# Kernel optimization log

Measured on AMD Instinct MI355X. Metric: run time of the kernel, lower is better.

The kernel has to match this reference:

```python
import jax, jax.numpy as jnp
import numpy as np

B, D, H, O, C, L = 16384, 1024, 1024, 256, 8, 3  # batch, input, hidden, output, num_classes, num_layers


def setup_inputs() -> dict:
    key = jax.random.key(0)
    ks = jax.random.split(key, 9)
    s_in = 1.0 / np.sqrt(D)
    s_h = 1.0 / np.sqrt(H)
    return {
        "x": jax.random.normal(ks[0], (B, D), jnp.float32),
        # classifier: Linear(D, C)
        "Wc": jax.random.normal(ks[1], (D, C), jnp.float32) * s_in,
        "bc": jnp.zeros((C,), jnp.float32),
        # per-branch first linear: Linear(D, H), stacked over C branches
        "W1": jax.random.normal(ks[2], (C, D, H), jnp.float32) * s_in,
        "b1": jnp.zeros((C, H), jnp.float32),
        # per-branch hidden linears: (num_layers-1) x Linear(H, H)
        "W2": jax.random.normal(ks[3], (C, L - 1, H, H), jnp.float32) * s_h,
        "b2": jnp.zeros((C, L - 1, H), jnp.float32),
        # per-branch output linear: Linear(H, O)
        "Wo": jax.random.normal(ks[4], (C, H, O), jnp.float32) * s_h,
        "bo": jnp.zeros((C, O), jnp.float32),
    }


def reference(x, Wc, bc, W1, b1, W2, b2, Wo, bo):
    # classifier logits: (B, C)
    logits = x @ Wc + bc
    # argmax routing (no target_bin given), clamped as in torch
    class_idx = jnp.clip(jnp.argmax(logits, axis=-1), 0, C - 1)
    one_hot = jax.nn.one_hot(class_idx, C, dtype=x.dtype)  # (B, C)
    # dense compute-all-branches, faithful to the torch module
    h = jax.nn.relu(jnp.einsum("bd,cdh->bch", x, W1) + b1)  # (B, C, H)
    for i in range(L - 1):
        h = jax.nn.relu(jnp.einsum("bch,chk->bck", h, W2[:, i]) + b2[:, i])
    outputs = jnp.einsum("bch,cho->bco", h, Wo) + bo  # (B, C, O)
    output = jnp.sum(one_hot[:, :, None] * outputs, axis=1)  # (B, O)
    return output, logits
```

## Files before the change

kernel.cpp:

```cpp
#include <hip/hip_runtime.h>
#include <stdint.h>

#define BB 16384
#define DD 1024
#define HH 1024
#define OO 256
#define CC 8

typedef unsigned short u16;
typedef __attribute__((ext_vector_type(4))) unsigned short u16x4;
typedef __attribute__((ext_vector_type(8))) short bf16x8;
typedef __attribute__((ext_vector_type(4))) float f32x4;

__device__ __forceinline__ u16 f2bf(float f) {
    union { float f; uint32_t u; } v; v.f = f;
    const uint32_t u = v.u;
    return (u16)((u + 0x7FFFu + ((u >> 16) & 1u)) >> 16);
}

#define GLDS16(g, l)                                                                   \
    __builtin_amdgcn_global_load_lds((const __attribute__((address_space(1))) void*)(g), \
                                     (__attribute__((address_space(3))) void*)(l), 16, 0, 0)

__global__ __launch_bounds__(256)
void transpose_bf16_kernel(const float* __restrict__ src, u16* __restrict__ dst,
                           int R, int Cc)
{
    __shared__ float t[32][33];
    const int tid = threadIdx.x;
    const int mat = blockIdx.z;
    const int r0 = blockIdx.y * 32, c0 = blockIdx.x * 32;
    {
        const int rr = tid >> 3, c4 = (tid & 7) * 4;
        const float4 v = *(const float4*)(src + ((size_t)mat * R + r0 + rr) * Cc + c0 + c4);
        t[rr][c4 + 0] = v.x; t[rr][c4 + 1] = v.y; t[rr][c4 + 2] = v.z; t[rr][c4 + 3] = v.w;
    }
    __syncthreads();
    {
        const int cc = tid >> 3, k4 = (tid & 7) * 4;
        u16x4 o;
        o[0] = f2bf(t[k4 + 0][cc]);
        o[1] = f2bf(t[k4 + 1][cc]);
        o[2] = f2bf(t[k4 + 2][cc]);
        o[3] = f2bf(t[k4 + 3][cc]);
        *(u16x4*)(dst + ((size_t)mat * Cc + c0 + cc) * R + r0 + k4) = o;
    }
}

__global__ __launch_bounds__(256)
void logits_kernel(const float* __restrict__ x, const float* __restrict__ Wc,
                   const float* __restrict__ bc, float* __restrict__ logits_out,
                   u16* __restrict__ x_bf16, int* __restrict__ class_idx,
                   int* __restrict__ hist)
{
    __shared__ float WcT[CC][DD];
    __shared__ int clsarr[16];
    const int tid = threadIdx.x;
    #pragma unroll
    for (int j = 0; j < 8; ++j) {
        const int f = tid + 256 * j;
        const float4 v = ((const float4*)Wc)[f];
        const int d = f >> 1, c = (f & 1) * 4;
        WcT[c + 0][d] = v.x; WcT[c + 1][d] = v.y; WcT[c + 2][d] = v.z; WcT[c + 3][d] = v.w;
    }
    __syncthreads();

    const int lane = tid & 63, wv = tid >> 6;
    const int row0 = blockIdx.x * 16 + wv * 4;

    float acc[4][8];
    #pragma unroll
    for (int r = 0; r < 4; ++r)
        #pragma unroll
        for (int c = 0; c < 8; ++c) acc[r][c] = 0.f;

    #pragma unroll
    for (int p = 0; p < 2; ++p) {
        float4 xv[2][4];
        #pragma unroll
        for (int rr = 0; rr < 2; ++rr) {
            const float4* xr = (const float4*)(x + (size_t)(row0 + 2 * p + rr) * DD);
            #pragma unroll
            for (int j = 0; j < 4; ++j) xv[rr][j] = xr[lane + 64 * j];
        }
        #pragma unroll
        for (int rr = 0; rr < 2; ++rr) {
            u16* xb = x_bf16 + (size_t)(row0 + 2 * p + rr) * DD;
            #pragma unroll
            for (int j = 0; j < 4; ++j) {
                const float4 v = xv[rr][j];
                u16x4 o; o[0] = f2bf(v.x); o[1] = f2bf(v.y); o[2] = f2bf(v.z); o[3] = f2bf(v.w);
                *(u16x4*)(xb + 4 * (lane + 64 * j)) = o;
            }
        }
        #pragma unroll
        for (int j = 0; j < 4; ++j) {
            const int f = lane + 64 * j;
            #pragma unroll
            for (int c = 0; c < 8; ++c) {
                const float4 w = *(const float4*)&WcT[c][4 * f];
                #pragma unroll
                for (int rr = 0; rr < 2; ++rr)
                    acc[2 * p + rr][c] += xv[rr][j].x * w.x + xv[rr][j].y * w.y
                                        + xv[rr][j].z * w.z + xv[rr][j].w * w.w;
            }
        }
    }

    #pragma unroll
    for (int off = 8; off < 64; off <<= 1)
        #pragma unroll
        for (int r = 0; r < 4; ++r)
            #pragma unroll
            for (int c = 0; c < 8; ++c)
                acc[r][c] += __shfl_xor(acc[r][c], off, 64);

    const int cls = lane >> 3;
    const float bcv = bc[cls];
    float s[4];
    #pragma unroll
    for (int r = 0; r < 4; ++r) {
        float v = acc[r][0];
        #pragma unroll
        for (int c = 1; c < 8; ++c) v = (cls == c) ? acc[r][c] : v;
        s[r] = v;
    }
    #pragma unroll
    for (int off = 1; off < 8; off <<= 1)
        #pragma unroll
        for (int r = 0; r < 4; ++r) s[r] += __shfl_xor(s[r], off, 64);
    #pragma unroll
    for (int r = 0; r < 4; ++r) s[r] += bcv;

    #pragma unroll
    for (int r = 0; r < 4; ++r)
        if ((lane & 7) == 0) logits_out[(size_t)(row0 + r) * CC + cls] = s[r];

    int idx[4] = {cls, cls, cls, cls};
    #pragma unroll
    for (int off = 8; off < 64; off <<= 1) {
        #pragma unroll
        for (int r = 0; r < 4; ++r) {
            const float ov = __shfl_xor(s[r], off, 64);
            const int oi = __shfl_xor(idx[r], off, 64);
            const bool take = (ov > s[r]) || (ov == s[r] && oi < idx[r]);
            s[r] = take ? ov : s[r];
            idx[r] = take ? oi : idx[r];
        }
    }
    if (lane == 0) {
        #pragma unroll
        for (int r = 0; r < 4; ++r) {
            class_idx[row0 + r] = idx[r];
            clsarr[wv * 4 + r] = idx[r];
        }
    }
    __syncthreads();
    if (tid < 64) {
        const int myc = (tid < 16) ? clsarr[tid] : -1;
        int h = 0;
        #pragma unroll
        for (int cc = 0; cc < 8; ++cc) {
            const int p = __popcll(__ballot(myc == cc));
            h = (tid == cc) ? p : h;
        }
        if (tid < 8) hist[blockIdx.x * 8 + tid] = h;
    }
}

__global__ __launch_bounds__(256)
void scan_kernel(const int* __restrict__ hist, int* __restrict__ offsets,
                 int* __restrict__ bb)
{
    const int t = threadIdx.x, c = t >> 5, g = t & 31;
    int sum = 0;
    #pragma unroll 4
    for (int i = 0; i < 32; ++i) sum += hist[(g * 32 + i) * 8 + c];
    int inc = sum;
    #pragma unroll
    for (int d = 1; d < 32; d <<= 1) {
        const int v = __shfl_up(inc, d, 32);
        if (g >= d) inc += v;
    }
    __shared__ int tot[8], offL[9];
    if (g == 31) tot[c] = inc;
    __syncthreads();
    if (t == 0) {
        int o = 0; offL[0] = 0; offsets[0] = 0;
        #pragma unroll
        for (int c8 = 0; c8 < 8; ++c8) {
            o += (tot[c8] + 127) & ~127;
            offL[c8 + 1] = o; offsets[c8 + 1] = o;
        }
    }
    __syncthreads();
    int base = offL[c] + (inc - sum);
    #pragma unroll 4
    for (int i = 0; i < 32; ++i) {
        const int b = g * 32 + i;
        bb[b * 8 + c] = base;
        base += hist[b * 8 + c];
    }
}

__global__ __launch_bounds__(256)
void scatter_kernel(const int* __restrict__ class_idx, const int* __restrict__ bb,
                    int* __restrict__ rowidx)
{
    const int r = blockIdx.x * 256 + threadIdx.x;
    const int c = class_idx[r];
    const int lane = threadIdx.x & 63;
    const int gl = lane & ~15;
    const unsigned long long before = (1ull << lane) - (1ull << gl);
    int rank = 0;
    #pragma unroll
    for (int cc = 0; cc < 8; ++cc) {
        const unsigned long long m = __ballot(c == cc);
        const int p = __popcll(m & before);
        rank = (c == cc) ? p : rank;
    }
    rowidx[bb[(r >> 4) * 8 + c] + rank] = r;
}

#define STAGE(b, kt)                            \
    {                                           \
        const int kb_ = (kt) * 32;              \
        GLDS16(gA0 + kb_, lA0 + (b) * 4096);    \
        GLDS16(gA1 + kb_, lA1 + (b) * 4096);    \
        GLDS16(gB0 + kb_, lB0 + (b) * 4096);    \
        GLDS16(gB1 + kb_, lB1 + (b) * 4096);    \
    }

#define COMPUTE(b)                                                        \
    {                                                                     \
        bf16x8 af[4], bfr[4];                                             \
        _Pragma("unroll")                                                 \
        for (int i = 0; i < 4; ++i) {                                     \
            af[i]  = *(const bf16x8*)(fA + (b) * 4096 + i * 16 * 32);     \
            bfr[i] = *(const bf16x8*)(fB + (b) * 4096 + i * 16 * 32);     \
        }                                                                 \
        __builtin_amdgcn_s_setprio(1);                                    \
        _Pragma("unroll")                                                 \
        for (int mi = 0; mi < 4; ++mi)                                    \
            _Pragma("unroll")                                             \
            for (int ni = 0; ni < 4; ++ni)                                \
                acc[mi][ni] = __builtin_amdgcn_mfma_f32_16x16x32_bf16(    \
                    af[mi], bfr[ni], acc[mi][ni], 0, 0, 0);               \
        __builtin_amdgcn_s_setprio(0);                                    \
    }

#define WAITV(N)                                                          \
    asm volatile("s_waitcnt vmcnt(" #N ")" ::: "memory");                 \
    __builtin_amdgcn_s_barrier();                                         \
    __builtin_amdgcn_sched_barrier(0);

template<int NT_Y, int NSTRIDE, bool GATHER_A, bool RELU, bool FINAL>
__global__ __launch_bounds__(256, 3)
void gemm_kernel(const u16* __restrict__ Abase, const u16* __restrict__ Wbase,
                 size_t wclass_stride, const float* __restrict__ bias_base,
                 int bias_stride, const int* __restrict__ offsets,
                 const int* __restrict__ rowidx, u16* __restrict__ Hout,
                 float* __restrict__ Fout)
{
    __shared__ u16 sA[3 * 128 * 32];
    __shared__ u16 sB[3 * 128 * 32];
    const int tid = threadIdx.x;

    const int bid = blockIdx.x;
    const int wg = (bid & 7) * ((int)gridDim.x >> 3) + (bid >> 3);
    const int m0 = (wg / NT_Y) * 128;
    const int n0 = (wg % NT_Y) * 128;
    if (m0 >= offsets[CC]) return;
    int c = 0;
    while (m0 >= offsets[c + 1]) ++c;

    const int srow = tid >> 2;
    const int kc8 = (tid & 3) * 8;
    int sa0 = m0 + srow, sa1 = m0 + srow + 64;
    if (GATHER_A) {
        const int g0 = rowidx[sa0]; sa0 = (g0 < 0) ? 0 : g0;
        const int g1 = rowidx[sa1]; sa1 = (g1 < 0) ? 0 : g1;
    }
    const u16* gA0 = Abase + (size_t)sa0 * 1024 + kc8;
    const u16* gA1 = Abase + (size_t)sa1 * 1024 + kc8;
    const u16* Wcl = Wbase + (size_t)c * wclass_stride;
    const u16* gB0 = Wcl + (size_t)(n0 + srow) * 1024 + kc8;
    const u16* gB1 = Wcl + (size_t)(n0 + srow + 64) * 1024 + kc8;
    u16* lA0 = sA + tid * 8;
    u16* lA1 = sA + 2048 + tid * 8;
    u16* lB0 = sB + tid * 8;
    u16* lB1 = sB + 2048 + tid * 8;

    const int lane = tid & 63, wv = tid >> 6;
    const int wm = (wv & 1) * 64, wn = (wv >> 1) * 64;
    const int lr = lane & 15, lg = lane >> 4;
    const u16* fA = sA + (wm + lr) * 32 + lg * 8;
    const u16* fB = sB + (wn + lr) * 32 + lg * 8;

    f32x4 acc[4][4];
    #pragma unroll
    for (int i = 0; i < 4; ++i)
        #pragma unroll
        for (int j = 0; j < 4; ++j)
            acc[i][j] = (f32x4){0.f, 0.f, 0.f, 0.f};

    STAGE(0, 0);
    STAGE(1, 1);
    for (int kt = 0; kt < 30; kt += 3) {
        WAITV(4);
        STAGE(2, kt + 2);
        COMPUTE(0);
        WAITV(4);
        STAGE(0, kt + 3);
        COMPUTE(1);
        WAITV(4);
        STAGE(1, kt + 4);
        COMPUTE(2);
    }
    WAITV(4);
    COMPUTE(0);
    WAITV(0);
    COMPUTE(1);

    const float* bp = bias_base + (size_t)c * bias_stride + n0 + wn + lr;
    #pragma unroll
    for (int ni = 0; ni < 4; ++ni) {
        const float bv = bp[ni * 16];
        const int col = n0 + wn + ni * 16 + lr;
        #pragma unroll
        for (int mi = 0; mi < 4; ++mi) {
            const int rb = m0 + wm + mi * 16 + lg * 4;
            #pragma unroll
            for (int q = 0; q < 4; ++q) {
                float v = acc[mi][ni][q] + bv;
                if (RELU) v = v > 0.f ? v : 0.f;
                if (FINAL) {
                    const int orow = rowidx[rb + q];
                    if (orow >= 0) Fout[(size_t)orow * NSTRIDE + col] = v;
                } else {
                    Hout[(size_t)(rb + q) * NSTRIDE + col] = f2bf(v);
                }
            }
        }
    }
}

extern "C" void kernel_launch(void* const* d_in, const int* in_sizes, int n_in,
                              void* d_out, int out_size, void* d_ws, size_t ws_size,
                              hipStream_t stream)
{
    const float* x  = (const float*)d_in[0];
    const float* Wc = (const float*)d_in[1];
    const float* bc = (const float*)d_in[2];
    const float* W1 = (const float*)d_in[3];
    const float* b1 = (const float*)d_in[4];
    const float* W2 = (const float*)d_in[5];
    const float* b2 = (const float*)d_in[6];
    const float* Wo = (const float*)d_in[7];
    const float* bo = (const float*)d_in[8];
    float* out    = (float*)d_out;
    float* logits = out + (size_t)BB * OO;

    char* ws = (char*)d_ws;
    constexpr size_t PADMAX = BB + CC * 128;
    constexpr int NLB = BB / 16;
    int* offsets   = (int*)(ws + 0);
    int* hist      = (int*)(ws + 64);
    int* bb        = (int*)(ws + 64 + NLB * 32);
    int* class_idx = (int*)(ws + 64 + 2 * NLB * 32);
    int* rowidx    = (int*)((char*)class_idx + (size_t)BB * 4);
    u16* x_bf16    = (u16*)((char*)rowidx + PADMAX * 4);
    u16* hA  = x_bf16 + (size_t)BB * DD;
    u16* hB  = hA + PADMAX * HH;
    u16* W1T = hB + PADMAX * HH;
    u16* W2T = W1T + (size_t)CC * DD * HH;
    u16* WoT = W2T + (size_t)CC * 2 * HH * HH;

    hipMemsetAsync(rowidx, 0xFF, PADMAX * 4, stream);

    transpose_bf16_kernel<<<dim3(32, 32, 8),  256, 0, stream>>>(W1, W1T, DD, HH);
    transpose_bf16_kernel<<<dim3(32, 32, 16), 256, 0, stream>>>(W2, W2T, HH, HH);
    transpose_bf16_kernel<<<dim3(8, 32, 8),   256, 0, stream>>>(Wo, WoT, HH, OO);

    logits_kernel<<<NLB, 256, 0, stream>>>(x, Wc, bc, logits, x_bf16, class_idx, hist);
    scan_kernel<<<1, 256, 0, stream>>>(hist, offsets, bb);
    scatter_kernel<<<BB / 256, 256, 0, stream>>>(class_idx, bb, rowidx);

    constexpr int MT = BB / 128 + CC;
    gemm_kernel<8, HH, true,  true,  false><<<dim3(MT * 8), 256, 0, stream>>>(
        x_bf16, W1T, (size_t)DD * HH, b1, HH, offsets, rowidx, hA, nullptr);
    gemm_kernel<8, HH, false, true,  false><<<dim3(MT * 8), 256, 0, stream>>>(
        hA, W2T, (size_t)2 * HH * HH, b2, 2 * HH, offsets, rowidx, hB, nullptr);
    gemm_kernel<8, HH, false, true,  false><<<dim3(MT * 8), 256, 0, stream>>>(
        hB, W2T + (size_t)HH * HH, (size_t)2 * HH * HH, b2 + HH, 2 * HH, offsets, rowidx, hA, nullptr);
    gemm_kernel<2, OO, false, false, true ><<<dim3(MT * 2), 256, 0, stream>>>(
        hA, WoT, (size_t)OO * HH, bo, OO, offsets, rowidx, nullptr, out);
}
```

Measured before the change: 273.8 us.

## Use 256x128 tiles with warp-specialized loaders and swizzled LDS for hidden GEMMs

Replaces the 128x128 hidden-layer GEMM with a 256x128 tile kernel, padding class segments to 256 rows. Two waves load A and two load B into an XOR-swizzled LDS layout, and each wave computes a 128x64 sub-tile with 8x4 MFMA accumulators. The larger tile is meant to raise arithmetic intensity and cut per-tile weight reloads, while the swizzle targets LDS bank conflicts. The cost is more registers and lower occupancy (launch bounds of 2), plus extra padded rows per class.

```diff
diff --git a/kernel.cpp b/kernel.cpp
--- a/kernel.cpp
+++ b/kernel.cpp
@@ -189,7 +189,7 @@
         int o = 0; offL[0] = 0; offsets[0] = 0;
         #pragma unroll
         for (int c8 = 0; c8 < 8; ++c8) {
-            o += (tot[c8] + 127) & ~127;
+            o += (tot[c8] + 255) & ~255;
             offL[c8 + 1] = o; offsets[c8 + 1] = o;
         }
     }
@@ -220,6 +220,139 @@
         rank = (c == cc) ? p : rank;
     }
     rowidx[bb[(r >> 4) * 8 + c] + rank] = r;
+}
+
+#define ABUF 8192
+#define BBUF 4096
+
+template<bool GATHER_A>
+__global__ __launch_bounds__(256, 2)
+void gemm256_kernel(const u16* __restrict__ Abase, const u16* __restrict__ Wbase,
+                    size_t wclass_stride, const float* __restrict__ bias_base,
+                    int bias_stride, const int* __restrict__ offsets,
+                    const int* __restrict__ rowidx, u16* __restrict__ Hout)
+{
+    __shared__ u16 sA[3 * ABUF];
+    __shared__ u16 sB[3 * BBUF];
+    const int tid = threadIdx.x;
+
+    const int bid = blockIdx.x;
+    const int wg = (bid & 7) * ((int)gridDim.x >> 3) + (bid >> 3);
+    const int m0 = (wg >> 3) * 256;
+    const int n0 = (wg & 7) * 128;
+    if (m0 >= offsets[CC]) return;
+    int c = 0;
+    while (m0 >= offsets[c + 1]) ++c;
+
+    const int wv = tid >> 6, ln = tid & 63;
+    const bool isA = (wv == 1 || wv == 2);
+    const int nGld = isA ? 8 : 4;
+    const int chunkBase = isA ? ((wv - 1) * 512) : ((wv == 3) ? 256 : 0);
+    const int bufStep = isA ? ABUF : BBUF;
+    u16* const ldsBase = isA ? sA : sB;
+    const u16* const Wcl = Wbase + (size_t)c * wclass_stride;
+
+    const u16* gsrc[8];
+    u16* ldst[8];
+    #pragma unroll
+    for (int j = 0; j < 8; ++j) {
+        if (j < nGld) {
+            const int n = chunkBase + j * 64 + ln;
+            const int row = n >> 2;
+            const int logc = (n & 3) ^ ((row >> 1) & 3);
+            ldst[j] = ldsBase + n * 8;
+            if (isA) {
+                int grow = m0 + row;
+                if (GATHER_A) { const int g = rowidx[grow]; grow = (g < 0) ? 0 : g; }
+                gsrc[j] = Abase + (size_t)grow * 1024 + logc * 8;
+            } else {
+                gsrc[j] = Wcl + (size_t)(n0 + row) * 1024 + logc * 8;
+            }
+        } else { gsrc[j] = nullptr; ldst[j] = nullptr; }
+    }
+
+    const int wm = wv >> 1, wn = wv & 1, lr = ln & 15, lg = ln >> 4;
+    const int arow0 = wm * 128 + lr;
+    const int brow0 = wn * 64 + lr;
+    const int pcA = lg ^ ((arow0 >> 1) & 3);
+    const int pcB = lg ^ ((brow0 >> 1) & 3);
+    const u16* const fA = sA + arow0 * 32 + pcA * 8;
+    const u16* const fB = sB + brow0 * 32 + pcB * 8;
+
+    f32x4 acc[8][4];
+    #pragma unroll
+    for (int i = 0; i < 8; ++i)
+        #pragma unroll
+        for (int j = 0; j < 4; ++j)
+            acc[i][j] = (f32x4){0.f, 0.f, 0.f, 0.f};
+
+#define STAGE6(KT, P)                                                     \
+    {                                                                     \
+        _Pragma("unroll")                                                 \
+        for (int j = 0; j < 8; ++j)                                       \
+            if (j < nGld) GLDS16(gsrc[j] + (KT) * 32, ldst[j] + (P) * bufStep); \
+    }
+
+#define COMPUTE6(P)                                                       \
+    {                                                                     \
+        bf16x8 bfr[4];                                                    \
+        _Pragma("unroll")                                                 \
+        for (int ni = 0; ni < 4; ++ni)                                    \
+            bfr[ni] = *(const bf16x8*)(fB + (P) * BBUF + ni * 512);       \
+        __builtin_amdgcn_s_setprio(1);                                    \
+        _Pragma("unroll")                                                 \
+        for (int mi = 0; mi < 8; ++mi) {                                  \
+            const bf16x8 a = *(const bf16x8*)(fA + (P) * ABUF + mi * 512);\
+            _Pragma("unroll")                                             \
+            for (int ni = 0; ni < 4; ++ni)                                \
+                acc[mi][ni] = __builtin_amdgcn_mfma_f32_16x16x32_bf16(    \
+                    a, bfr[ni], acc[mi][ni], 0, 0, 0);                    \
+        }                                                                 \
+        __builtin_amdgcn_s_setprio(0);                                    \
+    }
+
+#define BODY6(T, P, PN)                                                   \
+    {                                                                     \
+        STAGE6((T) + 1, (PN));                                            \
+        if (isA) asm volatile("s_waitcnt vmcnt(8)" ::: "memory");         \
+        else     asm volatile("s_waitcnt vmcnt(4)" ::: "memory");         \
+        __builtin_amdgcn_s_barrier();                                     \
+        __builtin_amdgcn_sched_barrier(0);                                \
+        COMPUTE6(P);                                                      \
+    }
+
+    STAGE6(0, 0);
+    for (int tb = 0; tb < 30; tb += 3) {
+        BODY6(tb + 0, 0, 1);
+        BODY6(tb + 1, 1, 2);
+        BODY6(tb + 2, 2, 0);
+    }
+    BODY6(30, 0, 1);
+    asm volatile("s_waitcnt vmcnt(0)" ::: "memory");
+    __builtin_amdgcn_s_barrier();
+    __builtin_amdgcn_sched_barrier(0);
+    COMPUTE6(1);
+
+#undef BODY6
+#undef COMPUTE6
+#undef STAGE6
+
+    const float* bp = bias_base + (size_t)c * bias_stride + n0 + wn * 64 + lr;
+    #pragma unroll
+    for (int ni = 0; ni < 4; ++ni) {
+        const float bv = bp[ni * 16];
+        const int col = n0 + wn * 64 + ni * 16 + lr;
+        #pragma unroll
+        for (int mi = 0; mi < 8; ++mi) {
+            const int rb = m0 + wm * 128 + mi * 16 + lg * 4;
+            #pragma unroll
+            for (int q = 0; q < 4; ++q) {
+                float v = acc[mi][ni][q] + bv;
+                v = v > 0.f ? v : 0.f;
+                Hout[(size_t)(rb + q) * HH + col] = f2bf(v);
+            }
+        }
+    }
 }
 
 #define STAGE(b, kt)                            \
@@ -254,13 +387,11 @@
     __builtin_amdgcn_s_barrier();                                         \
     __builtin_amdgcn_sched_barrier(0);
 
-template<int NT_Y, int NSTRIDE, bool GATHER_A, bool RELU, bool FINAL>
 __global__ __launch_bounds__(256, 3)
-void gemm_kernel(const u16* __restrict__ Abase, const u16* __restrict__ Wbase,
-                 size_t wclass_stride, const float* __restrict__ bias_base,
-                 int bias_stride, const int* __restrict__ offsets,
-                 const int* __restrict__ rowidx, u16* __restrict__ Hout,
-                 float* __restrict__ Fout)
+void gemm_final_kernel(const u16* __restrict__ Abase, const u16* __restrict__ Wbase,
+                       size_t wclass_stride, const float* __restrict__ bias_base,
+                       int bias_stride, const int* __restrict__ offsets,
+                       const int* __restrict__ rowidx, float* __restrict__ Fout)
 {
     __shared__ u16 sA[3 * 128 * 32];
     __shared__ u16 sB[3 * 128 * 32];
@@ -268,19 +399,15 @@
 
     const int bid = blockIdx.x;
     const int wg = (bid & 7) * ((int)gridDim.x >> 3) + (bid >> 3);
-    const int m0 = (wg / NT_Y) * 128;
-    const int n0 = (wg % NT_Y) * 128;
+    const int m0 = (wg >> 1) * 128;
+    const int n0 = (wg & 1) * 128;
     if (m0 >= offsets[CC]) return;
     int c = 0;
     while (m0 >= offsets[c + 1]) ++c;
 
     const int srow = tid >> 2;
     const int kc8 = (tid & 3) * 8;
-    int sa0 = m0 + srow, sa1 = m0 + srow + 64;
-    if (GATHER_A) {
-        const int g0 = rowidx[sa0]; sa0 = (g0 < 0) ? 0 : g0;
-        const int g1 = rowidx[sa1]; sa1 = (g1 < 0) ? 0 : g1;
-    }
+    const int sa0 = m0 + srow, sa1 = m0 + srow + 64;
     const u16* gA0 = Abase + (size_t)sa0 * 1024 + kc8;
     const u16* gA1 = Abase + (size_t)sa1 * 1024 + kc8;
     const u16* Wcl = Wbase + (size_t)c * wclass_stride;
@@ -332,14 +459,9 @@
             const int rb = m0 + wm + mi * 16 + lg * 4;
             #pragma unroll
             for (int q = 0; q < 4; ++q) {
-                float v = acc[mi][ni][q] + bv;
-                if (RELU) v = v > 0.f ? v : 0.f;
-                if (FINAL) {
-                    const int orow = rowidx[rb + q];
-                    if (orow >= 0) Fout[(size_t)orow * NSTRIDE + col] = v;
-                } else {
-                    Hout[(size_t)(rb + q) * NSTRIDE + col] = f2bf(v);
-                }
+                const float v = acc[mi][ni][q] + bv;
+                const int orow = rowidx[rb + q];
+                if (orow >= 0) Fout[(size_t)orow * OO + col] = v;
             }
         }
     }
@@ -362,7 +484,7 @@
     float* logits = out + (size_t)BB * OO;
 
     char* ws = (char*)d_ws;
-    constexpr size_t PADMAX = BB + CC * 128;
+    constexpr size_t PADMAX = BB + CC * 256;
     constexpr int NLB = BB / 16;
     int* offsets   = (int*)(ws + 0);
     int* hist      = (int*)(ws + 64);
@@ -386,13 +508,14 @@
     scan_kernel<<<1, 256, 0, stream>>>(hist, offsets, bb);
     scatter_kernel<<<BB / 256, 256, 0, stream>>>(class_idx, bb, rowidx);
 
-    constexpr int MT = BB / 128 + CC;
-    gemm_kernel<8, HH, true,  true,  false><<<dim3(MT * 8), 256, 0, stream>>>(
-        x_bf16, W1T, (size_t)DD * HH, b1, HH, offsets, rowidx, hA, nullptr);
-    gemm_kernel<8, HH, false, true,  false><<<dim3(MT * 8), 256, 0, stream>>>(
-        hA, W2T, (size_t)2 * HH * HH, b2, 2 * HH, offsets, rowidx, hB, nullptr);
-    gemm_kernel<8, HH, false, true,  false><<<dim3(MT * 8), 256, 0, stream>>>(
-        hB, W2T + (size_t)HH * HH, (size_t)2 * HH * HH, b2 + HH, 2 * HH, offsets, rowidx, hA, nullptr);
-    gemm_kernel<2, OO, false, false, true ><<<dim3(MT * 2), 256, 0, stream>>>(
-        hA, WoT, (size_t)OO * HH, bo, OO, offsets, rowidx, nullptr, out);
-}
+    constexpr int MT2 = (int)(PADMAX / 256);
+    constexpr int MT4 = (int)(PADMAX / 128);
+    gemm256_kernel<true ><<<dim3(MT2 * 8), 256, 0, stream>>>(
+        x_bf16, W1T, (size_t)DD * HH, b1, HH, offsets, rowidx, hA);
+    gemm256_kernel<false><<<dim3(MT2 * 8), 256, 0, stream>>>(
+        hA, W2T, (size_t)2 * HH * HH, b2, 2 * HH, offsets, rowidx, hB);
+    gemm256_kernel<false><<<dim3(MT2 * 8), 256, 0, stream>>>(
+        hB, W2T + (size_t)HH * HH, (size_t)2 * HH * HH, b2 + HH, 2 * HH, offsets, rowidx, hA);
+    gemm_final_kernel<<<dim3(MT4 * 2), 256, 0, stream>>>(
+        hA, WoT, (size_t)OO * HH, bo, OO, offsets, rowidx, out);
+}
```

Result: slower. 369.0 us (+34.8%).

## Use BK=64 double-buffered XOR-swizzled LDS tiles for hidden-layer GEMMs

Applied to the files above, without the earlier changes.

Splits the hidden-layer GEMMs into a new kernel that stages 128x64 K-tiles with double buffering instead of 128x32 triple buffering. The LDS layout is XOR-swizzled per row to avoid bank conflicts on fragment reads. Barriers become plain __syncthreads, and the occupancy hint of 3 blocks is dropped. The final output GEMM keeps the old pipeline as a separate kernel. The larger tile halves the number of barrier iterations but uses more LDS per block, which may reduce occupancy and leaves less prefetch depth to hide load latency.

```diff
diff --git a/kernel.cpp b/kernel.cpp
--- a/kernel.cpp
+++ b/kernel.cpp
@@ -222,7 +222,129 @@
     rowidx[bb[(r >> 4) * 8 + c] + rank] = r;
 }
 
-#define STAGE(b, kt)                            \
+#define MF(a, b, c) __builtin_amdgcn_mfma_f32_16x16x32_bf16((a), (b), (c), 0, 0, 0)
+
+template<bool GATHER_A>
+__global__ __launch_bounds__(256)
+void gemm_kernel(const u16* __restrict__ Abase, const u16* __restrict__ Wbase,
+                 size_t wclass_stride, const float* __restrict__ bias_base,
+                 int bias_stride, const int* __restrict__ offsets,
+                 const int* __restrict__ rowidx, u16* __restrict__ Hout)
+{
+    __shared__ u16 sA[2 * 8192];
+    __shared__ u16 sB[2 * 8192];
+    const int tid = threadIdx.x;
+
+    const int bid = blockIdx.x;
+    const int wg = (bid & 7) * ((int)gridDim.x >> 3) + (bid >> 3);
+    const int m0 = (wg >> 3) * 128;
+    const int n0 = (wg & 7) * 128;
+    if (m0 >= offsets[CC]) return;
+    int c = 0;
+    while (m0 >= offsets[c + 1]) ++c;
+
+    const u16* const Wcl = Wbase + (size_t)c * wclass_stride;
+
+    const u16* gsA[4]; const u16* gsB[4];
+    int dn[4];
+    #pragma unroll
+    for (int j = 0; j < 4; ++j) {
+        const int n = tid + 256 * j;
+        const int row = n >> 3;
+        const int logc = (n & 7) ^ (row & 7);
+        int grow = m0 + row;
+        if (GATHER_A) { const int g = rowidx[grow]; grow = (g < 0) ? 0 : g; }
+        gsA[j] = Abase + (size_t)grow * 1024 + logc * 8;
+        gsB[j] = Wcl + (size_t)(n0 + row) * 1024 + logc * 8;
+        dn[j] = n * 8;
+    }
+
+#define STAGE(SB, KT)                                                     \
+    { GLDS16(gsA[0] + (KT) * 64, sA + (SB) * 8192 + dn[0]);               \
+      GLDS16(gsA[1] + (KT) * 64, sA + (SB) * 8192 + dn[1]);               \
+      GLDS16(gsA[2] + (KT) * 64, sA + (SB) * 8192 + dn[2]);               \
+      GLDS16(gsA[3] + (KT) * 64, sA + (SB) * 8192 + dn[3]);               \
+      GLDS16(gsB[0] + (KT) * 64, sB + (SB) * 8192 + dn[0]);               \
+      GLDS16(gsB[1] + (KT) * 64, sB + (SB) * 8192 + dn[1]);               \
+      GLDS16(gsB[2] + (KT) * 64, sB + (SB) * 8192 + dn[2]);               \
+      GLDS16(gsB[3] + (KT) * 64, sB + (SB) * 8192 + dn[3]); }
+
+    const int wv = tid >> 6, ln = tid & 63;
+    const int wm = (wv & 1) * 64, wn = (wv >> 1) * 64;
+    const int lr = ln & 15, lg = ln >> 4;
+    const int s7 = lr & 7;
+    const int pc0 = ((0 * 4 + lg) ^ s7) * 8;
+    const int pc1 = ((1 * 4 + lg) ^ s7) * 8;
+    const u16* const fA = sA + (wm + lr) * 64;
+    const u16* const fB = sB + (wn + lr) * 64;
+
+    f32x4 acc[4][4];
+    #pragma unroll
+    for (int i = 0; i < 4; ++i)
+        #pragma unroll
+        for (int j = 0; j < 4; ++j)
+            acc[i][j] = (f32x4){0.f, 0.f, 0.f, 0.f};
+
+#define COMPUTE(SB)                                                       \
+    {                                                                     \
+        bf16x8 a0[4], b0[4], a1[4], b1[4];                                \
+        _Pragma("unroll")                                                 \
+        for (int i = 0; i < 4; ++i) {                                     \
+            a0[i] = *(const bf16x8*)(fA + (SB) * 8192 + i * 1024 + pc0);  \
+            b0[i] = *(const bf16x8*)(fB + (SB) * 8192 + i * 1024 + pc0);  \
+        }                                                                 \
+        __builtin_amdgcn_s_setprio(1);                                    \
+        _Pragma("unroll")                                                 \
+        for (int mi = 0; mi < 4; ++mi)                                    \
+            _Pragma("unroll")                                             \
+            for (int ni = 0; ni < 4; ++ni)                                \
+                acc[mi][ni] = MF(a0[mi], b0[ni], acc[mi][ni]);            \
+        __builtin_amdgcn_s_setprio(0);                                    \
+        _Pragma("unroll")                                                 \
+        for (int i = 0; i < 4; ++i) {                                     \
+            a1[i] = *(const bf16x8*)(fA + (SB) * 8192 + i * 1024 + pc1);  \
+            b1[i] = *(const bf16x8*)(fB + (SB) * 8192 + i * 1024 + pc1);  \
+        }                                                                 \
+        __builtin_amdgcn_s_setprio(1);                                    \
+        _Pragma("unroll")                                                 \
+        for (int mi = 0; mi < 4; ++mi)                                    \
+            _Pragma("unroll")                                             \
+            for (int ni = 0; ni < 4; ++ni)                                \
+                acc[mi][ni] = MF(a1[mi], b1[ni], acc[mi][ni]);            \
+        __builtin_amdgcn_s_setprio(0);                                    \
+    }
+
+    STAGE(0, 0);
+    __syncthreads();
+    for (int t = 0; t < 14; t += 2) {
+        STAGE(1, t + 1); COMPUTE(0); __syncthreads();
+        STAGE(0, t + 2); COMPUTE(1); __syncthreads();
+    }
+    STAGE(1, 15); COMPUTE(0); __syncthreads();
+    COMPUTE(1);
+
+#undef COMPUTE
+#undef STAGE
+
+    const float* bp = bias_base + (size_t)c * bias_stride + n0 + wn + lr;
+    #pragma unroll
+    for (int ni = 0; ni < 4; ++ni) {
+        const float bv = bp[ni * 16];
+        const int col = n0 + wn + ni * 16 + lr;
+        #pragma unroll
+        for (int mi = 0; mi < 4; ++mi) {
+            const int rb = m0 + wm + mi * 16 + lg * 4;
+            #pragma unroll
+            for (int q = 0; q < 4; ++q) {
+                float v = acc[mi][ni][q] + bv;
+                v = v > 0.f ? v : 0.f;
+                Hout[(size_t)(rb + q) * HH + col] = f2bf(v);
+            }
+        }
+    }
+}
+
+#define STAGE4(b, kt)                           \
     {                                           \
         const int kb_ = (kt) * 32;              \
         GLDS16(gA0 + kb_, lA0 + (b) * 4096);    \
@@ -231,7 +353,7 @@
         GLDS16(gB1 + kb_, lB1 + (b) * 4096);    \
     }
 
-#define COMPUTE(b)                                                        \
+#define COMPUTE4(b)                                                       \
     {                                                                     \
         bf16x8 af[4], bfr[4];                                             \
         _Pragma("unroll")                                                 \
@@ -254,13 +376,11 @@
     __builtin_amdgcn_s_barrier();                                         \
     __builtin_amdgcn_sched_barrier(0);
 
-template<int NT_Y, int NSTRIDE, bool GATHER_A, bool RELU, bool FINAL>
 __global__ __launch_bounds__(256, 3)
-void gemm_kernel(const u16* __restrict__ Abase, const u16* __restrict__ Wbase,
-                 size_t wclass_stride, const float* __restrict__ bias_base,
-                 int bias_stride, const int* __restrict__ offsets,
-                 const int* __restrict__ rowidx, u16* __restrict__ Hout,
-                 float* __restrict__ Fout)
+void gemm_final_kernel(const u16* __restrict__ Abase, const u16* __restrict__ Wbase,
+                       size_t wclass_stride, const float* __restrict__ bias_base,
+                       int bias_stride, const int* __restrict__ offsets,
+                       const int* __restrict__ rowidx, float* __restrict__ Fout)
 {
     __shared__ u16 sA[3 * 128 * 32];
     __shared__ u16 sB[3 * 128 * 32];
@@ -268,19 +388,15 @@
 
     const int bid = blockIdx.x;
     const int wg = (bid & 7) * ((int)gridDim.x >> 3) + (bid >> 3);
-    const int m0 = (wg / NT_Y) * 128;
-    const int n0 = (wg % NT_Y) * 128;
+    const int m0 = (wg >> 1) * 128;
+    const int n0 = (wg & 1) * 128;
     if (m0 >= offsets[CC]) return;
     int c = 0;
     while (m0 >= offsets[c + 1]) ++c;
 
     const int srow = tid >> 2;
     const int kc8 = (tid & 3) * 8;
-    int sa0 = m0 + srow, sa1 = m0 + srow + 64;
-    if (GATHER_A) {
-        const int g0 = rowidx[sa0]; sa0 = (g0 < 0) ? 0 : g0;
-        const int g1 = rowidx[sa1]; sa1 = (g1 < 0) ? 0 : g1;
-    }
+    const int sa0 = m0 + srow, sa1 = m0 + srow + 64;
     const u16* gA0 = Abase + (size_t)sa0 * 1024 + kc8;
     const u16* gA1 = Abase + (size_t)sa1 * 1024 + kc8;
     const u16* Wcl = Wbase + (size_t)c * wclass_stride;
@@ -304,23 +420,23 @@
         for (int j = 0; j < 4; ++j)
             acc[i][j] = (f32x4){0.f, 0.f, 0.f, 0.f};
 
-    STAGE(0, 0);
-    STAGE(1, 1);
+    STAGE4(0, 0);
+    STAGE4(1, 1);
     for (int kt = 0; kt < 30; kt += 3) {
         WAITV(4);
-        STAGE(2, kt + 2);
-        COMPUTE(0);
+        STAGE4(2, kt + 2);
+        COMPUTE4(0);
         WAITV(4);
-        STAGE(0, kt + 3);
-        COMPUTE(1);
+        STAGE4(0, kt + 3);
+        COMPUTE4(1);
         WAITV(4);
-        STAGE(1, kt + 4);
-        COMPUTE(2);
+        STAGE4(1, kt + 4);
+        COMPUTE4(2);
     }
     WAITV(4);
-    COMPUTE(0);
+    COMPUTE4(0);
     WAITV(0);
-    COMPUTE(1);
+    COMPUTE4(1);
 
     const float* bp = bias_base + (size_t)c * bias_stride + n0 + wn + lr;
     #pragma unroll
@@ -332,14 +448,9 @@
             const int rb = m0 + wm + mi * 16 + lg * 4;
             #pragma unroll
             for (int q = 0; q < 4; ++q) {
-                float v = acc[mi][ni][q] + bv;
-                if (RELU) v = v > 0.f ? v : 0.f;
-                if (FINAL) {
-                    const int orow = rowidx[rb + q];
-                    if (orow >= 0) Fout[(size_t)orow * NSTRIDE + col] = v;
-                } else {
-                    Hout[(size_t)(rb + q) * NSTRIDE + col] = f2bf(v);
-                }
+                const float v = acc[mi][ni][q] + bv;
+                const int orow = rowidx[rb + q];
+                if (orow >= 0) Fout[(size_t)orow * OO + col] = v;
             }
         }
     }
@@ -386,13 +497,13 @@
     scan_kernel<<<1, 256, 0, stream>>>(hist, offsets, bb);
     scatter_kernel<<<BB / 256, 256, 0, stream>>>(class_idx, bb, rowidx);
 
-    constexpr int MT = BB / 128 + CC;
-    gemm_kernel<8, HH, true,  true,  false><<<dim3(MT * 8), 256, 0, stream>>>(
-        x_bf16, W1T, (size_t)DD * HH, b1, HH, offsets, rowidx, hA, nullptr);
-    gemm_kernel<8, HH, false, true,  false><<<dim3(MT * 8), 256, 0, stream>>>(
-        hA, W2T, (size_t)2 * HH * HH, b2, 2 * HH, offsets, rowidx, hB, nullptr);
-    gemm_kernel<8, HH, false, true,  false><<<dim3(MT * 8), 256, 0, stream>>>(
-        hB, W2T + (size_t)HH * HH, (size_t)2 * HH * HH, b2 + HH, 2 * HH, offsets, rowidx, hA, nullptr);
-    gemm_kernel<2, OO, false, false, true ><<<dim3(MT * 2), 256, 0, stream>>>(
-        hA, WoT, (size_t)OO * HH, bo, OO, offsets, rowidx, nullptr, out);
-}
+    constexpr int MT = (int)(PADMAX / 128);
+    gemm_kernel<true ><<<dim3(MT * 8), 256, 0, stream>>>(
+        x_bf16, W1T, (size_t)DD * HH, b1, HH, offsets, rowidx, hA);
+    gemm_kernel<false><<<dim3(MT * 8), 256, 0, stream>>>(
+        hA, W2T, (size_t)2 * HH * HH, b2, 2 * HH, offsets, rowidx, hB);
+    gemm_kernel<false><<<dim3(MT * 8), 256, 0, stream>>>(
+        hB, W2T + (size_t)HH * HH, (size_t)2 * HH * HH, b2 + HH, 2 * HH, offsets, rowidx, hA);
+    gemm_final_kernel<<<dim3(MT * 2), 256, 0, stream>>>(
+        hA, WoT, (size_t)OO * HH, bo, OO, offsets, rowidx, out);
+}
```

New measurement: 320.2 us. 1.17x slower.
